# Optimization experiments

Hardware: AMD Instinct MI355X
Metric: run time of the kernel (lower is better)

## Reference

```python
import jax, jax.numpy as jnp
import numpy as np

B, D, N, S = 4096, 768, 8192, 4  # batch, embedding_dim, len(y)==cat rows, source_size


def setup_inputs() -> dict:
    key = jax.random.key(0)
    k1, k2, k3, k4 = jax.random.split(key, 4)
    batch_x = jax.random.normal(k1, (B, D), dtype=jnp.float32)
    cat = jax.random.normal(k2, (N, D), dtype=jnp.float32)
    y = jax.random.randint(k3, (N,), 0, 2, dtype=jnp.int32)
    # phi_srcs: xavier-uniform-like scale for (D, 1) params, stacked as [S, D]
    phi = jax.random.normal(k4, (S, D), dtype=jnp.float32) * 0.05
    bias = jnp.zeros((1,), dtype=jnp.float32)
    return {"batch_x": batch_x, "cat": cat, "y": y, "phi": phi, "bias": bias}


def reference(batch_x, cat, y, phi, bias):
    # con[n, b] = cat[n] . batch_x[b]   -> [N, B]
    con = jnp.einsum('nd,bd->nb', cat, batch_x)
    # F.normalize(con, p=4, dim=0): divide each column by its 4-norm (eps=1e-12)
    norm4 = jnp.power(jnp.sum(jnp.abs(con) ** 4, axis=0), 0.25)
    con = con / jnp.maximum(norm4, 1e-12)
    # softmax over all N rows (dim=0), per batch column
    con = jax.nn.softmax(con, axis=0)
    # chunk into S sources along the N axis: psi [S, N/S, B]
    psi = con.reshape(S, N // S, B)
    yf = y.astype(jnp.float32).reshape(S, N // S)  # y chunks [S, N/S]
    # theta_s = exp(x @ phi_s): [S, B]  (unnormalized, as in the original output path)
    theta = jnp.exp(jnp.einsum('bd,sd->sb', batch_x, phi))
    # per-source: sum_n y[s,n] * psi[s,n,b], then scale by theta[s,b]; sum over sources
    sum_matrix = jnp.sum(jnp.einsum('sn,snb->sb', yf, psi) * theta, axis=0)  # [B]
    y_hat = jax.nn.sigmoid(sum_matrix + bias)  # bias [1] broadcasts -> [B]
    return y_hat
```

## Files before the change

### kernel.cpp

```cpp
#include <hip/hip_runtime.h>
#include <hip/hip_bf16.h>
#include <stdint.h>

#define Bdim 4096
#define Ddim 768
#define Ndim 8192
#define Sdim 4

typedef __attribute__((ext_vector_type(8))) short short8;
typedef __attribute__((ext_vector_type(4))) float floatx4;

__device__ inline unsigned short f2bf(float f) {
  unsigned u = __builtin_bit_cast(unsigned, f);
  unsigned r = (u + 0x7fffu + ((u >> 16) & 1u)) >> 16;
  return (unsigned short)r;
}
__device__ inline float bf2f(unsigned short s) {
  return __builtin_bit_cast(float, (unsigned)s << 16);
}

__device__ inline void async_copy16(const void* g, void* l) {
  __builtin_amdgcn_global_load_lds(
      (__attribute__((address_space(1))) void*)(g),
      (__attribute__((address_space(3))) void*)(l),
      16, 0, 0);
}

__global__ void convert_kernel(const float* __restrict__ x,
                               const float* __restrict__ cat,
                               unsigned short* __restrict__ xb,
                               unsigned short* __restrict__ catb,
                               float* __restrict__ stats) {
  int gid = blockIdx.x * blockDim.x + threadIdx.x;
  int stride = gridDim.x * blockDim.x;
  const int nx4 = (Bdim * Ddim) / 4;
  const int nc4 = (Ndim * Ddim) / 4;
  for (int i = gid; i < nx4; i += stride) {
    float4 v = ((const float4*)x)[i];
    ushort4 o;
    o.x = f2bf(v.x); o.y = f2bf(v.y); o.z = f2bf(v.z); o.w = f2bf(v.w);
    ((ushort4*)xb)[i] = o;
  }
  for (int i = gid; i < nc4; i += stride) {
    float4 v = ((const float4*)cat)[i];
    ushort4 o;
    o.x = f2bf(v.x); o.y = f2bf(v.y); o.z = f2bf(v.z); o.w = f2bf(v.w);
    ((ushort4*)catb)[i] = o;
  }
  if (gid < 6 * Bdim) stats[gid] = 0.0f;
}

__global__ __launch_bounds__(256) void gemm_bt_kernel(
    const unsigned short* __restrict__ A,
    const unsigned short* __restrict__ Bm,
    unsigned short* __restrict__ C,
    float* __restrict__ s4) {
  __shared__ unsigned short As[128 * 32];
  __shared__ unsigned short Bs[128 * 32];

  const int tid = threadIdx.x;
  const int wave = tid >> 6;
  const int lane = tid & 63;
  const int quad = lane >> 4;
  const int l16 = lane & 15;
  const int wm = (wave & 1) * 64;
  const int wn = (wave >> 1) * 64;
  const int m0 = blockIdx.x * 128;
  const int n0 = blockIdx.y * 128;

  floatx4 acc[4][4];
#pragma unroll
  for (int i = 0; i < 4; ++i)
#pragma unroll
    for (int j = 0; j < 4; ++j) acc[i][j] = (floatx4){0.f, 0.f, 0.f, 0.f};

  const int c0 = tid, c1 = tid + 256;
  const int r0 = c0 >> 2, r1 = c1 >> 2;
  const int j0 = (c0 & 3) ^ (r0 & 3) ^ ((r0 >> 2) & 3);
  const int j1 = (c1 & 3) ^ (r1 & 3) ^ ((r1 >> 2) & 3);
  const unsigned short* a0 = A + (size_t)(m0 + r0) * Ddim + j0 * 8;
  const unsigned short* a1 = A + (size_t)(m0 + r1) * Ddim + j1 * 8;
  const unsigned short* b0 = Bm + (size_t)(n0 + r0) * Ddim + j0 * 8;
  const unsigned short* b1 = Bm + (size_t)(n0 + r1) * Ddim + j1 * 8;

  const int fl = (l16 & 3) ^ ((l16 >> 2) & 3);
  const int ksw = (quad ^ fl) * 8;

  for (int k0 = 0; k0 < Ddim; k0 += 32) {
    async_copy16(a0 + k0, (char*)As + c0 * 16);
    async_copy16(a1 + k0, (char*)As + c1 * 16);
    async_copy16(b0 + k0, (char*)Bs + c0 * 16);
    async_copy16(b1 + k0, (char*)Bs + c1 * 16);
    __syncthreads();

    short8 af[4], bf[4];
#pragma unroll
    for (int mi = 0; mi < 4; ++mi)
      af[mi] = *(const short8*)(As + (wm + mi * 16 + l16) * 32 + ksw);
#pragma unroll
    for (int ni = 0; ni < 4; ++ni)
      bf[ni] = *(const short8*)(Bs + (wn + ni * 16 + l16) * 32 + ksw);
#pragma unroll
    for (int mi = 0; mi < 4; ++mi)
#pragma unroll
      for (int ni = 0; ni < 4; ++ni)
        acc[mi][ni] = __builtin_amdgcn_mfma_f32_16x16x32_bf16(
            af[mi], bf[ni], acc[mi][ni], 0, 0, 0);
    __syncthreads();
  }

  float cs4[4] = {0.f, 0.f, 0.f, 0.f};
#pragma unroll
  for (int mi = 0; mi < 4; ++mi)
#pragma unroll
    for (int ni = 0; ni < 4; ++ni) {
      int row = m0 + wm + mi * 16 + quad * 4;
      int col = n0 + wn + ni * 16 + l16;
#pragma unroll
      for (int r = 0; r < 4; ++r) {
        float c = acc[mi][ni][r];
        C[(size_t)(row + r) * Bdim + col] = f2bf(c);
        float c2 = c * c;
        cs4[ni] += c2 * c2;
      }
    }
#pragma unroll
  for (int ni = 0; ni < 4; ++ni) {
    float v = cs4[ni];
    v += __shfl_xor(v, 16);
    v += __shfl_xor(v, 32);
    if (quad == 0) atomicAdd(&s4[n0 + wn + ni * 16 + l16], v);
  }
}

__global__ void expsum_kernel(const unsigned short* __restrict__ con,
                              const float* __restrict__ s4,
                              const int* __restrict__ y,
                              float* __restrict__ denom,
                              float* __restrict__ numer) {
  int col0 = blockIdx.x * 1024 + threadIdx.x * 4;
  int n0 = blockIdx.y * 64;
  int src = n0 / (Ndim / Sdim);

  float4 s = *(const float4*)(s4 + col0);
  float inv0 = 1.0f / fmaxf(sqrtf(sqrtf(s.x)), 1e-12f);
  float inv1 = 1.0f / fmaxf(sqrtf(sqrtf(s.y)), 1e-12f);
  float inv2 = 1.0f / fmaxf(sqrtf(sqrtf(s.z)), 1e-12f);
  float inv3 = 1.0f / fmaxf(sqrtf(sqrtf(s.w)), 1e-12f);

  const unsigned short* p = con + (size_t)n0 * Bdim + col0;
  float d0 = 0.f, d1 = 0.f, d2 = 0.f, d3 = 0.f;
  float m0 = 0.f, m1 = 0.f, m2 = 0.f, m3 = 0.f;
#pragma unroll 8
  for (int i = 0; i < 64; ++i) {
    ushort4 v = *(const ushort4*)(p + (size_t)i * Bdim);
    float yv = (float)y[n0 + i];
    float e0 = __expf(bf2f(v.x) * inv0);
    float e1 = __expf(bf2f(v.y) * inv1);
    float e2 = __expf(bf2f(v.z) * inv2);
    float e3 = __expf(bf2f(v.w) * inv3);
    d0 += e0; d1 += e1; d2 += e2; d3 += e3;
    m0 += e0 * yv; m1 += e1 * yv; m2 += e2 * yv; m3 += e3 * yv;
  }
  atomicAdd(&denom[col0 + 0], d0);
  atomicAdd(&denom[col0 + 1], d1);
  atomicAdd(&denom[col0 + 2], d2);
  atomicAdd(&denom[col0 + 3], d3);
  float* np = numer + (size_t)src * Bdim + col0;
  atomicAdd(np + 0, m0);
  atomicAdd(np + 1, m1);
  atomicAdd(np + 2, m2);
  atomicAdd(np + 3, m3);
}

__global__ void finalize_kernel(const float* __restrict__ x,
                                const float* __restrict__ phi,
                                const float* __restrict__ denom,
                                const float* __restrict__ numer,
                                const float* __restrict__ bias,
                                float* __restrict__ out) {
  int gw = (blockIdx.x * blockDim.x + threadIdx.x) >> 6;
  int lane = threadIdx.x & 63;
  if (gw >= Bdim) return;
  const float* xr = x + (size_t)gw * Ddim;
  float a0 = 0.f, a1 = 0.f, a2 = 0.f, a3 = 0.f;
  for (int d = lane; d < Ddim; d += 64) {
    float xv = xr[d];
    a0 = fmaf(xv, phi[d], a0);
    a1 = fmaf(xv, phi[Ddim + d], a1);
    a2 = fmaf(xv, phi[2 * Ddim + d], a2);
    a3 = fmaf(xv, phi[3 * Ddim + d], a3);
  }
#pragma unroll
  for (int off = 32; off > 0; off >>= 1) {
    a0 += __shfl_down(a0, off);
    a1 += __shfl_down(a1, off);
    a2 += __shfl_down(a2, off);
    a3 += __shfl_down(a3, off);
  }
  if (lane == 0) {
    float s = numer[gw] * __expf(a0) + numer[Bdim + gw] * __expf(a1) +
              numer[2 * Bdim + gw] * __expf(a2) + numer[3 * Bdim + gw] * __expf(a3);
    s = s / denom[gw];
    float z = s + bias[0];
    out[gw] = 1.0f / (1.0f + __expf(-z));
  }
}

extern "C" void kernel_launch(void* const* d_in, const int* in_sizes, int n_in,
                              void* d_out, int out_size, void* d_ws,
                              size_t ws_size, hipStream_t stream) {
  const float* batch_x = (const float*)d_in[0];
  const float* cat = (const float*)d_in[1];
  const int* y = (const int*)d_in[2];
  const float* phi = (const float*)d_in[3];
  const float* bias = (const float*)d_in[4];
  float* out = (float*)d_out;

  char* ws = (char*)d_ws;
  unsigned short* catb = (unsigned short*)ws;
  unsigned short* xb = catb + (size_t)Ndim * Ddim;
  unsigned short* con = xb + (size_t)Bdim * Ddim;
  float* stats = (float*)(con + (size_t)Ndim * Bdim);
  float* s4 = stats;
  float* denom = s4 + Bdim;
  float* numer = denom + Bdim;

  convert_kernel<<<2048, 256, 0, stream>>>(batch_x, cat, xb, catb, stats);

  dim3 g2(Ndim / 128, Bdim / 128);
  gemm_bt_kernel<<<g2, 256, 0, stream>>>(catb, xb, con, s4);

  dim3 g3(Bdim / 1024, Ndim / 64);
  expsum_kernel<<<g3, 256, 0, stream>>>(con, s4, y, denom, numer);

  finalize_kernel<<<1024, 256, 0, stream>>>(batch_x, phi, denom, numer, bias, out);
}
```

Baseline: 193.0 us.

## Fuse finalize into expsum tail and precompute theta in convert; drop LDS swizzle

Computes theta = exp(x·phi) inside the conversion kernel and replaces the separate finalize kernel with a last-block-done epilogue in expsum, guarded by an atomic counter. This removes one kernel launch and the finalize pass. The GEMM's XOR swizzle on LDS tile addresses is also removed in favour of plain row-major indexing, which simplifies addressing but can reintroduce LDS bank conflicts on the fragment reads.

```diff
diff --git a/kernel.cpp b/kernel.cpp
--- a/kernel.cpp
+++ b/kernel.cpp
@@ -28,9 +28,11 @@
 
 __global__ void convert_kernel(const float* __restrict__ x,
                                const float* __restrict__ cat,
+                               const float* __restrict__ phi,
                                unsigned short* __restrict__ xb,
                                unsigned short* __restrict__ catb,
-                               float* __restrict__ stats) {
+                               float* __restrict__ stats,
+                               float* __restrict__ theta) {
   int gid = blockIdx.x * blockDim.x + threadIdx.x;
   int stride = gridDim.x * blockDim.x;
   const int nx4 = (Bdim * Ddim) / 4;
@@ -47,7 +49,34 @@
     o.x = f2bf(v.x); o.y = f2bf(v.y); o.z = f2bf(v.z); o.w = f2bf(v.w);
     ((ushort4*)catb)[i] = o;
   }
-  if (gid < 6 * Bdim) stats[gid] = 0.0f;
+  if (gid < 6 * Bdim + 256) stats[gid] = 0.0f;
+
+  int gw = gid >> 6;
+  int lane = threadIdx.x & 63;
+  if (gw < Bdim) {
+    const float* xr = x + (size_t)gw * Ddim;
+    float a0 = 0.f, a1 = 0.f, a2 = 0.f, a3 = 0.f;
+    for (int d = lane; d < Ddim; d += 64) {
+      float xv = xr[d];
+      a0 = fmaf(xv, phi[d], a0);
+      a1 = fmaf(xv, phi[Ddim + d], a1);
+      a2 = fmaf(xv, phi[2 * Ddim + d], a2);
+      a3 = fmaf(xv, phi[3 * Ddim + d], a3);
+    }
+#pragma unroll
+    for (int off = 32; off > 0; off >>= 1) {
+      a0 += __shfl_down(a0, off);
+      a1 += __shfl_down(a1, off);
+      a2 += __shfl_down(a2, off);
+      a3 += __shfl_down(a3, off);
+    }
+    if (lane == 0) {
+      theta[gw] = __expf(a0);
+      theta[Bdim + gw] = __expf(a1);
+      theta[2 * Bdim + gw] = __expf(a2);
+      theta[3 * Bdim + gw] = __expf(a3);
+    }
+  }
 }
 
 __global__ __launch_bounds__(256) void gemm_bt_kernel(
@@ -75,16 +104,12 @@
     for (int j = 0; j < 4; ++j) acc[i][j] = (floatx4){0.f, 0.f, 0.f, 0.f};
 
   const int c0 = tid, c1 = tid + 256;
-  const int r0 = c0 >> 2, r1 = c1 >> 2;
-  const int j0 = (c0 & 3) ^ (r0 & 3) ^ ((r0 >> 2) & 3);
-  const int j1 = (c1 & 3) ^ (r1 & 3) ^ ((r1 >> 2) & 3);
-  const unsigned short* a0 = A + (size_t)(m0 + r0) * Ddim + j0 * 8;
-  const unsigned short* a1 = A + (size_t)(m0 + r1) * Ddim + j1 * 8;
-  const unsigned short* b0 = Bm + (size_t)(n0 + r0) * Ddim + j0 * 8;
-  const unsigned short* b1 = Bm + (size_t)(n0 + r1) * Ddim + j1 * 8;
-
-  const int fl = (l16 & 3) ^ ((l16 >> 2) & 3);
-  const int ksw = (quad ^ fl) * 8;
+  const int r0 = c0 >> 2, col0 = (c0 & 3) * 8;
+  const int r1 = c1 >> 2, col1 = (c1 & 3) * 8;
+  const unsigned short* a0 = A + (size_t)(m0 + r0) * Ddim + col0;
+  const unsigned short* a1 = A + (size_t)(m0 + r1) * Ddim + col1;
+  const unsigned short* b0 = Bm + (size_t)(n0 + r0) * Ddim + col0;
+  const unsigned short* b1 = Bm + (size_t)(n0 + r1) * Ddim + col1;
 
   for (int k0 = 0; k0 < Ddim; k0 += 32) {
     async_copy16(a0 + k0, (char*)As + c0 * 16);
@@ -96,10 +121,10 @@
     short8 af[4], bf[4];
 #pragma unroll
     for (int mi = 0; mi < 4; ++mi)
-      af[mi] = *(const short8*)(As + (wm + mi * 16 + l16) * 32 + ksw);
+      af[mi] = *(const short8*)(As + (wm + mi * 16 + l16) * 32 + quad * 8);
 #pragma unroll
     for (int ni = 0; ni < 4; ++ni)
-      bf[ni] = *(const short8*)(Bs + (wn + ni * 16 + l16) * 32 + ksw);
+      bf[ni] = *(const short8*)(Bs + (wn + ni * 16 + l16) * 32 + quad * 8);
 #pragma unroll
     for (int mi = 0; mi < 4; ++mi)
 #pragma unroll
@@ -137,7 +162,11 @@
                               const float* __restrict__ s4,
                               const int* __restrict__ y,
                               float* __restrict__ denom,
-                              float* __restrict__ numer) {
+                              float* __restrict__ numer,
+                              const float* __restrict__ theta,
+                              const float* __restrict__ bias,
+                              int* __restrict__ counter,
+                              float* __restrict__ out) {
   int col0 = blockIdx.x * 1024 + threadIdx.x * 4;
   int n0 = blockIdx.y * 64;
   int src = n0 / (Ndim / Sdim);
@@ -171,39 +200,30 @@
   atomicAdd(np + 1, m1);
   atomicAdd(np + 2, m2);
   atomicAdd(np + 3, m3);
-}
-
-__global__ void finalize_kernel(const float* __restrict__ x,
-                                const float* __restrict__ phi,
-                                const float* __restrict__ denom,
-                                const float* __restrict__ numer,
-                                const float* __restrict__ bias,
-                                float* __restrict__ out) {
-  int gw = (blockIdx.x * blockDim.x + threadIdx.x) >> 6;
-  int lane = threadIdx.x & 63;
-  if (gw >= Bdim) return;
-  const float* xr = x + (size_t)gw * Ddim;
-  float a0 = 0.f, a1 = 0.f, a2 = 0.f, a3 = 0.f;
-  for (int d = lane; d < Ddim; d += 64) {
-    float xv = xr[d];
-    a0 = fmaf(xv, phi[d], a0);
-    a1 = fmaf(xv, phi[Ddim + d], a1);
-    a2 = fmaf(xv, phi[2 * Ddim + d], a2);
-    a3 = fmaf(xv, phi[3 * Ddim + d], a3);
-  }
-#pragma unroll
-  for (int off = 32; off > 0; off >>= 1) {
-    a0 += __shfl_down(a0, off);
-    a1 += __shfl_down(a1, off);
-    a2 += __shfl_down(a2, off);
-    a3 += __shfl_down(a3, off);
-  }
-  if (lane == 0) {
-    float s = numer[gw] * __expf(a0) + numer[Bdim + gw] * __expf(a1) +
-              numer[2 * Bdim + gw] * __expf(a2) + numer[3 * Bdim + gw] * __expf(a3);
-    s = s / denom[gw];
-    float z = s + bias[0];
-    out[gw] = 1.0f / (1.0f + __expf(-z));
+
+  __threadfence();
+  __syncthreads();
+  __shared__ int is_last;
+  if (threadIdx.x == 0) {
+    int old = atomicAdd(counter, 1);
+    is_last = (old == (int)(gridDim.x * gridDim.y) - 1);
+  }
+  __syncthreads();
+  if (is_last) {
+    float bv = bias[0];
+    for (int b = threadIdx.x; b < Bdim; b += 256) {
+      float den = __hip_atomic_load(&denom[b], __ATOMIC_RELAXED,
+                                    __HIP_MEMORY_SCOPE_AGENT);
+      float acc = 0.f;
+#pragma unroll
+      for (int si = 0; si < Sdim; ++si) {
+        float nu = __hip_atomic_load(&numer[si * Bdim + b], __ATOMIC_RELAXED,
+                                     __HIP_MEMORY_SCOPE_AGENT);
+        acc += nu * theta[si * Bdim + b];
+      }
+      float z = acc / den + bv;
+      out[b] = 1.0f / (1.0f + __expf(-z));
+    }
   }
 }
 
@@ -225,14 +245,16 @@
   float* s4 = stats;
   float* denom = s4 + Bdim;
   float* numer = denom + Bdim;
-
-  convert_kernel<<<2048, 256, 0, stream>>>(batch_x, cat, xb, catb, stats);
+  int* counter = (int*)(stats + 6 * Bdim);
+  float* theta = stats + 6 * Bdim + 256;
+
+  convert_kernel<<<2048, 256, 0, stream>>>(batch_x, cat, phi, xb, catb, stats,
+                                           theta);
 
   dim3 g2(Ndim / 128, Bdim / 128);
   gemm_bt_kernel<<<g2, 256, 0, stream>>>(catb, xb, con, s4);
 
   dim3 g3(Bdim / 1024, Ndim / 64);
-  expsum_kernel<<<g3, 256, 0, stream>>>(con, s4, y, denom, numer);
-
-  finalize_kernel<<<1024, 256, 0, stream>>>(batch_x, phi, denom, numer, bias, out);
-}
+  expsum_kernel<<<g3, 256, 0, stream>>>(con, s4, y, denom, numer, theta, bias,
+                                        counter, out);
+}
```

Result: slower. 215.2 us (+11.5%).
